# Kernel optimization log

Hardware: AMD Instinct MI355X
Metric: run time of the kernel (lower is better)

Reference implementation:

```python
import jax, jax.numpy as jnp
import numpy as np

B, Q, H, W, C = 2, 8192, 64, 64, 64
C9 = C * 9
EPS = 1e-6


def _mlp(x, params):
    # gelu MLP, no activation on last layer (matches repo mlp)
    for Wm, b in params[:-1]:
        x = jax.nn.gelu(x @ Wm + b)
    Wl, bl = params[-1]
    return x @ Wl + bl


def _make_coord(h, w):
    # pixel-center coords in (-1,1); channel 0 = row dim, channel 1 = col dim
    hs = -1.0 + (2.0 * jnp.arange(h, dtype=jnp.float32) + 1.0) / h
    ws = -1.0 + (2.0 * jnp.arange(w, dtype=jnp.float32) + 1.0) / w
    return jnp.stack(jnp.meshgrid(hs, ws, indexing='ij'), axis=0)  # (2,h,w)


def _nearest_gather(feat, coord):
    # F.grid_sample(mode='nearest', align_corners=False) on a (B,1,q,2) grid.
    # feat (B,C,H,W); coord (B,q,2) with [...,0] indexing H, [...,1] indexing W
    h, w = feat.shape[-2], feat.shape[-1]
    ih = jnp.clip(jnp.round((coord[..., 0] + 1.0) * h / 2.0 - 0.5), 0, h - 1).astype(jnp.int32)
    iw = jnp.clip(jnp.round((coord[..., 1] + 1.0) * w / 2.0 - 0.5), 0, w - 1).astype(jnp.int32)
    return jax.vmap(lambda f, a, b: f[:, a, b].T)(feat, ih, iw)  # (B,q,C)


def _unfold3(feat):
    # F.unfold(feat, 3, padding=1).view(B, C*9, H, W): channel-major, kernel row-major
    b, c, h, w = feat.shape
    p = jnp.pad(feat, ((0, 0), (0, 0), (1, 1), (1, 1)))
    patches = jnp.stack([p[:, :, i:i + h, j:j + w] for i in range(3) for j in range(3)], axis=2)
    return patches.reshape(b, c * 9, h, w)


def _forward(inp, coord, scale, enc_w, enc_b, iw0, ib0, iw1, ib1, iw2, ib2,
             sw0, sb0, sw1, sb1, ww0, wb0, ww1, wb1):
    # encoder (stand-in conv3x3, 3 -> C feature channels)
    feat = jax.lax.conv_general_dilated(inp, enc_w, (1, 1), 'SAME',
                                        dimension_numbers=('NCHW', 'OIHW', 'NCHW'))
    feat = feat + enc_b[None, :, None, None]
    feat = _unfold3(feat)  # (B, C*9, H, W)
    bsz, cf, h, w = feat.shape
    fcoord = jnp.broadcast_to(_make_coord(h, w)[None], (bsz, 2, h, w))
    dims = jnp.array([h, w], dtype=feat.dtype)

    tx = (h - 1) / (1.0 - scale[:, 0, 0])  # (B,)
    ty = (w - 1) / (1.0 - scale[:, 0, 1])
    rx, ry = 1.0 / tx, 1.0 / ty
    scale_tok = scale * dims  # (B,q,2)

    imnet_p = [(iw0, ib0), (iw1, ib1), (iw2, ib2)]
    score_p = [(sw0, sb0), (sw1, sb1)]
    weight_p = [(ww0, wb0), (ww1, wb1)]

    preds = []
    for vx in (-1, 1):
        for vy in (-1, 1):
            shift = jnp.stack([vx * rx + EPS, vy * ry + EPS], axis=-1)[:, None, :]  # (B,1,2)
            c = jnp.clip(coord + shift, -1.0 + 1e-6, 1.0 - 1e-6)
            value = _nearest_gather(feat, c)      # (B,q,C*9)
            coord_k = _nearest_gather(fcoord, c)  # (B,q,2)
            rel = (coord - coord_k) * dims        # (B,q,2)
            score = _mlp(rel, score_p)            # (B,q,1) -> broadcast over 3
            mlp_in = jnp.concatenate([rel, scale_tok], axis=-1)  # (B,q,4)
            wmat = _mlp(mlp_in, imnet_p).reshape(bsz, -1, cf, 3)  # (B,q,C*9,3)
            preds.append(jnp.einsum('bqc,bqck->bqk', value, wmat) + score)
    stacked = jnp.stack(preds, axis=-1)  # (B,q,3,4)
    return _mlp(stacked, weight_p)[..., 0]  # (B,q,3)


def setup_inputs() -> dict:
    key = jax.random.key(0)
    ks = jax.random.split(key, 16)
    f32 = jnp.float32

    def wi(k, shape, fan_in):
        return jax.random.normal(k, shape, f32) / np.float32(np.sqrt(fan_in))

    return {
        'inp': jax.random.normal(ks[0], (B, 3, H, W), f32),
        'coord': jax.random.uniform(ks[1], (B, Q, 2), f32, -1.0 + 1e-4, 1.0 - 1e-4),
        'scale': jax.random.uniform(ks[2], (B, Q, 2), f32, 0.01, 0.05),
        'enc_w': wi(ks[3], (C, 3, 3, 3), 27),
        'enc_b': jnp.zeros((C,), f32),
        'iw0': wi(ks[4], (4, 256), 4), 'ib0': jnp.zeros((256,), f32),
        'iw1': wi(ks[5], (256, 256), 256), 'ib1': jnp.zeros((256,), f32),
        'iw2': wi(ks[6], (256, C9 * 3), 256), 'ib2': jnp.zeros((C9 * 3,), f32),
        'sw0': wi(ks[7], (2, 256), 2), 'sb0': jnp.zeros((256,), f32),
        'sw1': wi(ks[8], (256, 1), 256), 'sb1': jnp.zeros((1,), f32),
        'ww0': wi(ks[9], (4, 256), 4), 'wb0': jnp.zeros((256,), f32),
        'ww1': wi(ks[10], (256, 1), 256), 'wb1': jnp.zeros((1,), f32),
    }


def reference(inp, coord, scale, enc_w, enc_b, iw0, ib0, iw1, ib1, iw2, ib2,
              sw0, sb0, sw1, sb1, ww0, wb0, ww1, wb1):
    return _forward(inp, coord, scale, enc_w, enc_b, iw0, ib0, iw1, ib1, iw2, ib2,
                    sw0, sb0, sw1, sb1, ww0, wb0, ww1, wb1)
```

## Files before the change

### kernel.cpp

```cpp
#include <hip/hip_runtime.h>

#define QN 8192
#define CCH 64
#define NROW 65536
#define MR 64
#define NBLK (NROW / MR)
#define H0S 264

typedef _Float16 f16x8 __attribute__((ext_vector_type(8)));
typedef _Float16 f16x4 __attribute__((ext_vector_type(4)));
typedef float f32x4 __attribute__((ext_vector_type(4)));

__device__ __forceinline__ float gelu_f(float x) {
    float x2 = x * x;
    float tt = fmaf(0.044715f, x2, 1.0f);
    float e = __expf(1.5957691216f * x * tt);
    float r = __builtin_amdgcn_rcpf(1.0f + e);
    return x - x * r;
}

__global__ __launch_bounds__(256) void k_pre(const float* __restrict__ inp,
                                             const float* __restrict__ ew,
                                             const float* __restrict__ eb,
                                             const float* __restrict__ coord,
                                             const float* __restrict__ scale,
                                             const float* __restrict__ sw0,
                                             const float* __restrict__ sb0,
                                             const float* __restrict__ sw1,
                                             const float* __restrict__ sb1,
                                             const float* __restrict__ iw1,
                                             const float* __restrict__ iw2,
                                             const float* __restrict__ ib2,
                                             float* __restrict__ featpad,
                                             float4* __restrict__ mlp_in,
                                             int2* __restrict__ ihiw,
                                             float* __restrict__ scoreg,
                                             _Float16* __restrict__ w1tp,
                                             _Float16* __restrict__ w2tp,
                                             float* __restrict__ b2p) {
    const int bb = blockIdx.x;
    const int tt0 = threadIdx.x;
    if (bb < 2178) {
        __shared__ float s_ew[1728];
        for (int i = tt0; i < 1728; i += 256) s_ew[i] = ew[i];
        __syncthreads();
        int idx = bb * 256 + tt0;
        const int total = 2 * 66 * 66 * CCH;
        if (idx >= total) return;
        int o = idx & 63; int pix = idx >> 6;
        int xx = pix % 66; int t2 = pix / 66;
        int yy = t2 % 66;  int b = t2 / 66;
        int y = yy - 1, x = xx - 1;
        float acc = 0.0f;
        if (y >= 0 && y < 64 && x >= 0 && x < 64) {
            acc = eb[o];
            for (int i = 0; i < 3; ++i) {
                const float* ip = inp + ((b * 3 + i) * 64) * 64;
                const float* wp = s_ew + (o * 3 + i) * 9;
                #pragma unroll
                for (int ky = 0; ky < 3; ++ky) {
                    int sy = y + ky - 1;
                    if (sy < 0 || sy > 63) continue;
                    #pragma unroll
                    for (int kx = 0; kx < 3; ++kx) {
                        int sx = x + kx - 1;
                        if (sx < 0 || sx > 63) continue;
                        acc += ip[sy * 64 + sx] * wp[ky * 3 + kx];
                    }
                }
            }
        }
        featpad[idx] = acc;
    } else if (bb < 2434) {
        int row = (bb - 2178) * 256 + tt0;
        int v = row & 3;
        int bq = row >> 2;
        int b = bq >> 13;
        float c0 = coord[bq * 2 + 0], c1 = coord[bq * 2 + 1];
        float s0 = scale[bq * 2 + 0], s1 = scale[bq * 2 + 1];
        float s00 = scale[(b * QN) * 2 + 0];
        float s01 = scale[(b * QN) * 2 + 1];
        float rx = (1.0f - s00) / 63.0f;
        float ry = (1.0f - s01) / 63.0f;
        float vx = (v & 2) ? 1.0f : -1.0f;
        float vy = (v & 1) ? 1.0f : -1.0f;
        float cc0 = c0 + vx * rx + 1e-6f;
        float cc1 = c1 + vy * ry + 1e-6f;
        cc0 = fminf(fmaxf(cc0, -1.0f + 1e-6f), 1.0f - 1e-6f);
        cc1 = fminf(fmaxf(cc1, -1.0f + 1e-6f), 1.0f - 1e-6f);
        int ih = (int)rintf((cc0 + 1.0f) * 32.0f - 0.5f);
        int iw = (int)rintf((cc1 + 1.0f) * 32.0f - 0.5f);
        ih = min(max(ih, 0), 63);
        iw = min(max(iw, 0), 63);
        float ck0 = (2.0f * (float)ih + 1.0f) / 64.0f - 1.0f;
        float ck1 = (2.0f * (float)iw + 1.0f) / 64.0f - 1.0f;
        float rel0 = (c0 - ck0) * 64.0f;
        float rel1 = (c1 - ck1) * 64.0f;
        mlp_in[row] = make_float4(rel0, rel1, s0 * 64.0f, s1 * 64.0f);
        ihiw[row] = make_int2(ih, iw);
        float sc = sb1[0];
        #pragma unroll 4
        for (int t2 = 0; t2 < 256; ++t2) {
            float h = gelu_f(fmaf(rel0, sw0[t2], fmaf(rel1, sw0[256 + t2], sb0[t2])));
            sc = fmaf(h, sw1[t2], sc);
        }
        scoreg[row] = sc;
    } else {
        int idx = (bb - 2434) * 256 + tt0;
        if (idx < 442368) {
            int j = idx & 7, ln = (idx >> 3) & 63, kf = (idx >> 9) & 7, tl = idx >> 12;
            int np = tl * 16 + (ln & 15);
            int kk = kf * 32 + (ln >> 4) * 8 + j;
            int k_out = np / 576;
            int rem = np - 576 * k_out;
            int tap = rem >> 6, cch = rem & 63;
            int n = (cch * 9 + tap) * 3 + k_out;
            w2tp[idx] = (_Float16)iw2[kk * 1728 + n];
            if (kf == 0 && j == 0 && (ln >> 4) == 0) b2p[np] = ib2[n];
        } else {
            int i2 = idx - 442368;
            int j = i2 & 7, ln = (i2 >> 3) & 63, kf = (i2 >> 9) & 7, ct = i2 >> 12;
            int col = ct * 16 + (ln & 15);
            int kk = kf * 32 + (ln >> 4) * 8 + j;
            w1tp[i2] = (_Float16)iw1[kk * 256 + col];
        }
    }
}

#define LDX1(B, CT) do { const _Float16* wp_ = w1tp + (size_t)((CT) * 8) * 512 + lane * 8;        \
    _Pragma("unroll") for (int kf_ = 0; kf_ < 4; ++kf_) B[kf_] = *(const f16x8*)(wp_ + kf_ * 512); } while (0)
#define LDY1(B, CT) do { const _Float16* wp_ = w1tp + (size_t)((CT) * 8 + 4) * 512 + lane * 8;    \
    _Pragma("unroll") for (int kf_ = 0; kf_ < 4; ++kf_) B[kf_] = *(const f16x8*)(wp_ + kf_ * 512); } while (0)
#define LDX2(B, TI) do { const _Float16* wp_ = w2tp + (size_t)((TI) * 8) * 512 + lane * 8;        \
    _Pragma("unroll") for (int kf_ = 0; kf_ < 4; ++kf_) B[kf_] = *(const f16x8*)(wp_ + kf_ * 512); } while (0)
#define LDY2(B, BV, TI) do { const _Float16* wp_ = w2tp + (size_t)((TI) * 8 + 4) * 512 + lane * 8;\
    _Pragma("unroll") for (int kf_ = 0; kf_ < 4; ++kf_) B[kf_] = *(const f16x8*)(wp_ + kf_ * 512);\
    BV = b2p[(TI) * 16 + l15]; } while (0)
#define ZACC() do { _Pragma("unroll") for (int rt_ = 0; rt_ < 4; ++rt_)                           \
    acc[rt_] = (f32x4){0.f, 0.f, 0.f, 0.f}; } while (0)
#define MFMAH(B, OFS) do { _Pragma("unroll") for (int kf_ = 0; kf_ < 4; ++kf_)                    \
    { _Pragma("unroll") for (int rt_ = 0; rt_ < 4; ++rt_)                                         \
      acc[rt_] = __builtin_amdgcn_mfma_f32_16x16x32_f16(a[rt_][kf_ + (OFS)], B[kf_], acc[rt_], 0, 0, 0); } } while (0)
#define H1EPI(CT) do { int col_ = (CT) * 16 + l15; float bias_ = ib1[col_];                       \
    _Pragma("unroll") for (int rt_ = 0; rt_ < 4; ++rt_)                                           \
      { _Pragma("unroll") for (int rg_ = 0; rg_ < 4; ++rg_)                                       \
        s_h0[(rt_ * 16 + quad * 4 + rg_) * H0S + col_] = (_Float16)gelu_f(acc[rt_][rg_] + bias_); } } while (0)
#define EPI3(TI, BV) do { int cf36_ = (TI) - ((TI) / 36) * 36;                                    \
    const _Float16* vb_ = s_valT + (cf36_ * 16 + l15) * 64;                                       \
    _Pragma("unroll") for (int rt_ = 0; rt_ < 4; ++rt_) {                                         \
      f16x4 vv_ = *(const f16x4*)(vb_ + ((rt_ * 16 + quad * 4) ^ swz));                           \
      _Pragma("unroll") for (int rg_ = 0; rg_ < 4; ++rg_)                                         \
        pA[rt_][rg_] = fmaf(acc[rt_][rg_] + (BV), (float)vv_[rg_], pA[rt_][rg_]); } } while (0)
#define FLUSH(KT) do { _Pragma("unroll") for (int rt_ = 0; rt_ < 4; ++rt_)                        \
    { _Pragma("unroll") for (int rg_ = 0; rg_ < 4; ++rg_) {                                       \
        float x_ = pA[rt_][rg_];                                                                  \
        _Pragma("unroll") for (int m_ = 1; m_ < 16; m_ <<= 1) x_ += __shfl_xor(x_, m_, 64);       \
        if (l15 == 0) atomicAdd(&s_pred[rt_ * 16 + quad * 4 + rg_][KT], x_);                      \
        pA[rt_][rg_] = 0.f; } } } while (0)

__global__ __launch_bounds__(256, 2) void k_fused(const float* __restrict__ featpad,
                                                  const float4* __restrict__ mlp_in,
                                                  const int2* __restrict__ ihiw,
                                                  const float* __restrict__ iw0,
                                                  const float* __restrict__ ib0,
                                                  const _Float16* __restrict__ w1tp,
                                                  const float* __restrict__ ib1,
                                                  const _Float16* __restrict__ w2tp,
                                                  const float* __restrict__ b2p,
                                                  const float* __restrict__ scoreg,
                                                  const float* __restrict__ ww0,
                                                  const float* __restrict__ wb0,
                                                  const float* __restrict__ ww1,
                                                  const float* __restrict__ wb1,
                                                  float* __restrict__ out) {
    __shared__ __align__(16) char pool[576 * 64 * 2];
    _Float16* s_h0   = (_Float16*)pool;
    _Float16* s_valT = (_Float16*)pool;
    __shared__ float4 s_min[MR];
    __shared__ int    s_base[MR];
    __shared__ int    s_dtab[9];
    __shared__ float  s_pred[MR][3];
    __shared__ float  s_score[MR];
    __shared__ float  s_wred[48][4];

    const int t = threadIdx.x;
    const int wave = t >> 6, lane = t & 63, quad = lane >> 4, l15 = lane & 15;
    const int rowbase = blockIdx.x * MR;

    if (t < MR) {
        int row = rowbase + t;
        s_min[t] = mlp_in[row];
        s_score[t] = scoreg[row];
        int b = row >> 15;
        int2 p = ihiw[row];
        s_base[t] = ((b * 66 + p.x) * 66 + p.y) * 64;
    }
    if (t < 9) { int di = t / 3; s_dtab[t] = (di * 66 + (t - 3 * di)) * 64; }
    if (t < MR * 3) s_pred[t / 3][t % 3] = 0.0f;
    __syncthreads();

    {
        float w0 = iw0[t], w1 = iw0[256 + t], w2 = iw0[512 + t], w3 = iw0[768 + t];
        float bb = ib0[t];
        #pragma unroll 4
        for (int r = 0; r < MR; ++r) {
            float4 m = s_min[r];
            s_h0[r * H0S + t] =
                (_Float16)gelu_f(fmaf(m.x, w0, fmaf(m.y, w1, fmaf(m.z, w2, fmaf(m.w, w3, bb)))));
        }
    }
    __syncthreads();

    f16x8 bX0[4], bX1[4], bY0[4], bY1[4];
    float bv0, bv1;
    f32x4 acc[4];
    const int w4 = wave * 4;
    const int tbase = wave * 27;

    LDX1(bX0, w4);
    LDY1(bY0, w4);
    LDX1(bX1, w4 + 1);

    f16x8 a[4][8];
    #pragma unroll
    for (int rt = 0; rt < 4; ++rt)
        #pragma unroll
        for (int kf = 0; kf < 8; ++kf)
            a[rt][kf] = *(const f16x8*)(s_h0 + (rt * 16 + l15) * H0S + kf * 32 + quad * 8);
    __syncthreads();

    LDY1(bY1, w4 + 1);
    ZACC(); MFMAH(bX0, 0);
    LDX1(bX0, w4 + 2);
    MFMAH(bY0, 4);
    H1EPI(w4);
    LDY1(bY0, w4 + 2);
    ZACC(); MFMAH(bX1, 0);
    LDX1(bX1, w4 + 3);
    MFMAH(bY1, 4);
    H1EPI(w4 + 1);
    LDY1(bY1, w4 + 3);
    ZACC(); MFMAH(bX0, 0);
    LDX2(bX0, tbase);
    MFMAH(bY0, 4);
    H1EPI(w4 + 2);
    LDY2(bY0, bv0, tbase);
    ZACC(); MFMAH(bX1, 0);
    LDX2(bX1, tbase + 1);
    MFMAH(bY1, 4);
    H1EPI(w4 + 3);
    __syncthreads();

    #pragma unroll
    for (int rt = 0; rt < 4; ++rt)
        #pragma unroll
        for (int kf = 0; kf < 8; ++kf)
            a[rt][kf] = *(const f16x8*)(s_h0 + (rt * 16 + l15) * H0S + kf * 32 + quad * 8);
    __syncthreads();

    #pragma unroll 1
    for (int g4 = 0; g4 < 9; ++g4) {
        float4 v[4];
        #pragma unroll
        for (int u = 0; u < 4; ++u) {
            int c4 = wave + (g4 * 4 + u) * 4;
            int tap = c4 >> 4;
            int cch0 = (c4 & 15) << 2;
            v[u] = *(const float4*)(featpad + s_base[lane] + s_dtab[tap] + cch0);
        }
        #pragma unroll
        for (int u = 0; u < 4; ++u) {
            int c4 = wave + (g4 * 4 + u) * 4;
            int cfp = c4 << 2;
            s_valT[(cfp + 0) * 64 + (lane ^ (((cfp + 0) & 7) << 3))] = (_Float16)v[u].x;
            s_valT[(cfp + 1) * 64 + (lane ^ (((cfp + 1) & 7) << 3))] = (_Float16)v[u].y;
            s_valT[(cfp + 2) * 64 + (lane ^ (((cfp + 2) & 7) << 3))] = (_Float16)v[u].z;
            s_valT[(cfp + 3) * 64 + (lane ^ (((cfp + 3) & 7) << 3))] = (_Float16)v[u].w;
        }
    }
    __syncthreads();

    const int kt0 = tbase / 36;
    int bsplit = (kt0 + 1) * 36 - tbase; if (bsplit > 27) bsplit = 27;
    const int ktB = (tbase + 26) / 36;
    const int swz = (l15 & 7) << 3;

    float pA[4][4];
    #pragma unroll
    for (int rt = 0; rt < 4; ++rt)
        #pragma unroll
        for (int rg = 0; rg < 4; ++rg) pA[rt][rg] = 0.f;

    #pragma unroll 1
    for (int p = 0; p < 13; ++p) {
        int i = 2 * p;
        int ti = tbase + i;
        LDY2(bY1, bv1, ti + 1);
        ZACC(); MFMAH(bX0, 0);
        LDX2(bX0, ti + 2);
        MFMAH(bY0, 4);
        EPI3(ti, bv0);
        if (i == bsplit - 1) FLUSH(kt0);
        LDY2(bY0, bv0, ti + 2);
        ZACC(); MFMAH(bX1, 0);
        if (p < 12) LDX2(bX1, ti + 3);
        MFMAH(bY1, 4);
        EPI3(ti + 1, bv1);
        if (i + 1 == bsplit - 1) FLUSH(kt0);
    }
    {
        ZACC(); MFMAH(bX0, 0); MFMAH(bY0, 4);
        EPI3(tbase + 26, bv0);
        if (26 == bsplit - 1) FLUSH(kt0);
    }
    FLUSH(ktB);
    __syncthreads();

    if (t < 192) {
        int o = t >> 2, sub = t & 3;
        int bql = o / 3, k = o - 3 * bql;
        float x0 = s_pred[bql * 4 + 0][k] + s_score[bql * 4 + 0];
        float x1 = s_pred[bql * 4 + 1][k] + s_score[bql * 4 + 1];
        float x2 = s_pred[bql * 4 + 2][k] + s_score[bql * 4 + 2];
        float x3 = s_pred[bql * 4 + 3][k] + s_score[bql * 4 + 3];
        float acc2 = 0.0f;
        int j0 = sub * 64;
        #pragma unroll 4
        for (int j = j0; j < j0 + 64; ++j) {
            float h = gelu_f(fmaf(x0, ww0[j], fmaf(x1, ww0[256 + j],
                          fmaf(x2, ww0[512 + j], fmaf(x3, ww0[768 + j], wb0[j])))));
            acc2 = fmaf(h, ww1[j], acc2);
        }
        s_wred[o][sub] = acc2;
    }
    __syncthreads();
    if (t < 48) {
        int bql = t / 3, k = t - 3 * bql;
        float r2 = s_wred[t][0] + s_wred[t][1] + s_wred[t][2] + s_wred[t][3] + wb1[0];
        out[(blockIdx.x * 16 + bql) * 3 + k] = r2;
    }
}

extern "C" void kernel_launch(void* const* d_in, const int* in_sizes, int n_in,
                              void* d_out, int out_size, void* d_ws, size_t ws_size,
                              hipStream_t stream) {
    const float* inp   = (const float*)d_in[0];
    const float* coord = (const float*)d_in[1];
    const float* scale = (const float*)d_in[2];
    const float* ew    = (const float*)d_in[3];
    const float* eb    = (const float*)d_in[4];
    const float* iw0   = (const float*)d_in[5];
    const float* ib0   = (const float*)d_in[6];
    const float* iw1   = (const float*)d_in[7];
    const float* ib1   = (const float*)d_in[8];
    const float* iw2   = (const float*)d_in[9];
    const float* ib2   = (const float*)d_in[10];
    const float* sw0   = (const float*)d_in[11];
    const float* sb0   = (const float*)d_in[12];
    const float* sw1   = (const float*)d_in[13];
    const float* sb1   = (const float*)d_in[14];
    const float* ww0   = (const float*)d_in[15];
    const float* wb0   = (const float*)d_in[16];
    const float* ww1   = (const float*)d_in[17];
    const float* wb1   = (const float*)d_in[18];
    float* out = (float*)d_out;

    char* ws = (char*)d_ws;
    float*     featpad = (float*)(ws + 0);
    float4*    mlp_in  = (float4*)(ws + 2230272);
    int2*      ihiw    = (int2*)(ws + 3278848);
    float*     scoreg  = (float*)(ws + 3803136);
    _Float16*  w1tp    = (_Float16*)(ws + 4065280);
    _Float16*  w2tp    = (_Float16*)(ws + 4196352);
    float*     b2p     = (float*)(ws + 5081088);

    k_pre<<<dim3(4418), dim3(256), 0, stream>>>(inp, ew, eb, coord, scale,
                                                sw0, sb0, sw1, sb1, iw1, iw2, ib2,
                                                featpad, mlp_in, ihiw, scoreg,
                                                w1tp, w2tp, b2p);
    k_fused<<<dim3(NBLK), dim3(256), 0, stream>>>(featpad, mlp_in, ihiw,
                                                  iw0, ib0, w1tp, ib1, w2tp, b2p,
                                                  scoreg, ww0, wb0, ww1, wb1, out);
}
```

Measured before the change: 236.8 us.

## Overlap unfold-value gather with second MLP GEMM via staged, rotated tile order

Replaces the up-front gather of the 576 neighbourhood feature values into shared memory with a staged load, one kernel row at a time, spread across the output-layer GEMM loop. Each wave starts its tile sequence at a rotated offset so it consumes only rows already in shared memory, and barriers are inserted at per-wave iteration points. The goal is to hide global gather latency behind MFMA work instead of stalling before the loop. The cost is extra barriers inside the hot loop, more live registers for the prefetched values, and intricate per-wave index bookkeeping that could break correctness if the barrier schedule is off.

```diff
diff --git a/kernel.cpp b/kernel.cpp
--- a/kernel.cpp
+++ b/kernel.cpp
@@ -145,8 +145,8 @@
     _Pragma("unroll") for (int rt_ = 0; rt_ < 4; ++rt_)                                           \
       { _Pragma("unroll") for (int rg_ = 0; rg_ < 4; ++rg_)                                       \
         s_h0[(rt_ * 16 + quad * 4 + rg_) * H0S + col_] = (_Float16)gelu_f(acc[rt_][rg_] + bias_); } } while (0)
-#define EPI3(TI, BV) do { int cf36_ = (TI) - ((TI) / 36) * 36;                                    \
-    const _Float16* vb_ = s_valT + (cf36_ * 16 + l15) * 64;                                       \
+#define EPI3(CF, BV) do {                                                                         \
+    const _Float16* vb_ = s_valT + ((CF) * 16 + l15) * 64;                                        \
     _Pragma("unroll") for (int rt_ = 0; rt_ < 4; ++rt_) {                                         \
       f16x4 vv_ = *(const f16x4*)(vb_ + ((rt_ * 16 + quad * 4) ^ swz));                           \
       _Pragma("unroll") for (int rg_ = 0; rg_ < 4; ++rg_)                                         \
@@ -157,6 +157,20 @@
         _Pragma("unroll") for (int m_ = 1; m_ < 16; m_ <<= 1) x_ += __shfl_xor(x_, m_, 64);       \
         if (l15 == 0) atomicAdd(&s_pred[rt_ * 16 + quad * 4 + rg_][KT], x_);                      \
         pA[rt_][rg_] = 0.f; } } } while (0)
+
+#define GLOADR(V, CH, B_) do { int dt_ = ((CH) * 66 + (B_)) * 64 + 4 * wave;                      \
+    _Pragma("unroll") for (int u_ = 0; u_ < 4; ++u_)                                              \
+        V[u_] = *(const float4*)(featpad + gbase + dt_ + 16 * u_); } while (0)
+#define GSTORER(V, CH, B_) do { int sw_ = 4 * (wave & 1);                                         \
+    _Pragma("unroll") for (int u_ = 0; u_ < 4; ++u_) {                                            \
+        int vb_ = (192 * (CH) + 64 * (B_) + 16 * u_ + 4 * wave) * 64;                             \
+        s_valT[vb_ +   0 + (lane ^ ((sw_ + 0) << 3))] = (_Float16)V[u_].x;                        \
+        s_valT[vb_ +  64 + (lane ^ ((sw_ + 1) << 3))] = (_Float16)V[u_].y;                        \
+        s_valT[vb_ + 128 + (lane ^ ((sw_ + 2) << 3))] = (_Float16)V[u_].z;                        \
+        s_valT[vb_ + 192 + (lane ^ ((sw_ + 3) << 3))] = (_Float16)V[u_].w;                        \
+    } } while (0)
+
+#define TIF(M) (tbase + ((i0 + (M)) >= 27 ? (i0 + (M) - 27) : (i0 + (M))))
 
 __global__ __launch_bounds__(256, 2) void k_fused(const float* __restrict__ featpad,
                                                   const float4* __restrict__ mlp_in,
@@ -178,7 +192,6 @@
     _Float16* s_valT = (_Float16*)pool;
     __shared__ float4 s_min[MR];
     __shared__ int    s_base[MR];
-    __shared__ int    s_dtab[9];
     __shared__ float  s_pred[MR][3];
     __shared__ float  s_score[MR];
     __shared__ float  s_wred[48][4];
@@ -195,7 +208,6 @@
         int2 p = ihiw[row];
         s_base[t] = ((b * 66 + p.x) * 66 + p.y) * 64;
     }
-    if (t < 9) { int di = t / 3; s_dtab[t] = (di * 66 + (t - 3 * di)) * 64; }
     if (t < MR * 3) s_pred[t / 3][t % 3] = 0.0f;
     __syncthreads();
 
@@ -211,11 +223,19 @@
     }
     __syncthreads();
 
+    const int w4 = wave * 4;
+    const int tbase = wave * 27;
+    const int i0    = (wave == 1) ? 9  : (wave == 2) ? 18 : 0;
+    const int s36   = (wave == 1) ? 27 : (wave == 2) ? 18 : (wave == 3) ? 9 : 0;
+    const int barA  = (wave == 2) ? 9  : (wave == 3) ? 3  : 12;
+    const int barB  = (wave == 0) ? 24 : (wave == 1) ? 18 : 15;
+    const int nwrap = 26 - i0;
+    const int ktA   = (wave == 0) ? 0 : (wave == 1) ? 1 : 2;
+    const int ktB   = (wave <= 1) ? 0 : (wave == 2) ? 1 : 2;
+
     f16x8 bX0[4], bX1[4], bY0[4], bY1[4];
     float bv0, bv1;
     f32x4 acc[4];
-    const int w4 = wave * 4;
-    const int tbase = wave * 27;
 
     LDX1(bX0, w4);
     LDY1(bY0, w4);
@@ -241,15 +261,20 @@
     H1EPI(w4 + 1);
     LDY1(bY1, w4 + 3);
     ZACC(); MFMAH(bX0, 0);
-    LDX2(bX0, tbase);
+    LDX2(bX0, TIF(0));
     MFMAH(bY0, 4);
     H1EPI(w4 + 2);
-    LDY2(bY0, bv0, tbase);
+    LDY2(bY0, bv0, TIF(0));
     ZACC(); MFMAH(bX1, 0);
-    LDX2(bX1, tbase + 1);
+    LDX2(bX1, TIF(1));
     MFMAH(bY1, 4);
     H1EPI(w4 + 3);
     __syncthreads();
+
+    float4 gA[4], gB[4];
+    const int gbase = s_base[lane];
+    GLOADR(gA, 0, 0);
+    GLOADR(gB, 0, 1);
 
     #pragma unroll
     for (int rt = 0; rt < 4; ++rt)
@@ -258,31 +283,12 @@
             a[rt][kf] = *(const f16x8*)(s_h0 + (rt * 16 + l15) * H0S + kf * 32 + quad * 8);
     __syncthreads();
 
-    #pragma unroll 1
-    for (int g4 = 0; g4 < 9; ++g4) {
-        float4 v[4];
-        #pragma unroll
-        for (int u = 0; u < 4; ++u) {
-            int c4 = wave + (g4 * 4 + u) * 4;
-            int tap = c4 >> 4;
-            int cch0 = (c4 & 15) << 2;
-            v[u] = *(const float4*)(featpad + s_base[lane] + s_dtab[tap] + cch0);
-        }
-        #pragma unroll
-        for (int u = 0; u < 4; ++u) {
-            int c4 = wave + (g4 * 4 + u) * 4;
-            int cfp = c4 << 2;
-            s_valT[(cfp + 0) * 64 + (lane ^ (((cfp + 0) & 7) << 3))] = (_Float16)v[u].x;
-            s_valT[(cfp + 1) * 64 + (lane ^ (((cfp + 1) & 7) << 3))] = (_Float16)v[u].y;
-            s_valT[(cfp + 2) * 64 + (lane ^ (((cfp + 2) & 7) << 3))] = (_Float16)v[u].z;
-            s_valT[(cfp + 3) * 64 + (lane ^ (((cfp + 3) & 7) << 3))] = (_Float16)v[u].w;
-        }
-    }
-    __syncthreads();
-
-    const int kt0 = tbase / 36;
-    int bsplit = (kt0 + 1) * 36 - tbase; if (bsplit > 27) bsplit = 27;
-    const int ktB = (tbase + 26) / 36;
+    GSTORER(gA, 0, 0);
+    GLOADR(gA, 0, 2);
+    GSTORER(gB, 0, 1);
+    GSTORER(gA, 0, 2);
+    __syncthreads();
+
     const int swz = (l15 & 7) << 3;
 
     float pA[4][4];
@@ -293,25 +299,39 @@
 
     #pragma unroll 1
     for (int p = 0; p < 13; ++p) {
-        int i = 2 * p;
-        int ti = tbase + i;
-        LDY2(bY1, bv1, ti + 1);
+        const int nE = 2 * p, nO = nE + 1;
+        if (nE == barA || nE == barB) __syncthreads();
+        if (p == 0) { GLOADR(gA, 1, 0); GLOADR(gB, 1, 1); }
+        else if (p == 2) { GLOADR(gA, 2, 0); }
+        else if (p == 3) { GSTORER(gA, 2, 1); GLOADR(gA, 2, 2); }
+        int iiE = i0 + nE; if (iiE >= 27) iiE -= 27;
+        int cfE = s36 + iiE; if (cfE >= 36) cfE -= 36;
+        LDY2(bY1, bv1, TIF(nE + 1));
         ZACC(); MFMAH(bX0, 0);
-        LDX2(bX0, ti + 2);
+        LDX2(bX0, TIF(nE + 2));
         MFMAH(bY0, 4);
-        EPI3(ti, bv0);
-        if (i == bsplit - 1) FLUSH(kt0);
-        LDY2(bY0, bv0, ti + 2);
+        EPI3(cfE, bv0);
+        if (p == 1) { GSTORER(gB, 1, 1); GSTORER(gA, 1, 2); }
+        if (nE == nwrap) FLUSH(ktA);
+        if (nO == barA || nO == barB) __syncthreads();
+        if (p == 0) { GSTORER(gA, 1, 0); GLOADR(gA, 1, 2); }
+        else if (p == 2) { GSTORER(gA, 2, 0); GLOADR(gA, 2, 1); }
+        else if (p == 3) { GSTORER(gA, 2, 2); }
+        int iiO = iiE + 1; if (iiO >= 27) iiO -= 27;
+        int cfO = s36 + iiO; if (cfO >= 36) cfO -= 36;
+        LDY2(bY0, bv0, TIF(nO + 1));
         ZACC(); MFMAH(bX1, 0);
-        if (p < 12) LDX2(bX1, ti + 3);
+        if (p < 12) LDX2(bX1, TIF(nO + 2));
         MFMAH(bY1, 4);
-        EPI3(ti + 1, bv1);
-        if (i + 1 == bsplit - 1) FLUSH(kt0);
+        EPI3(cfO, bv1);
+        if (nO == nwrap) FLUSH(ktA);
     }
     {
+        int iiT = i0 + 26; if (iiT >= 27) iiT -= 27;
+        int cfT = s36 + iiT; if (cfT >= 36) cfT -= 36;
         ZACC(); MFMAH(bX0, 0); MFMAH(bY0, 4);
-        EPI3(tbase + 26, bv0);
-        if (26 == bsplit - 1) FLUSH(kt0);
+        EPI3(cfT, bv0);
+        if (26 == nwrap) FLUSH(ktA);
     }
     FLUSH(ktB);
     __syncthreads();
```

New measurement: 430.8 us. +81.9%, slower.
